# Performance work log

Measured on AMD Instinct MI355X. Metric: run time of the kernel, lower is better.

The kernel has to match this reference:

```python
import jax, jax.numpy as jnp
import numpy as np

H = 16  # num heads
DH = 64  # head dim


def setup_inputs() -> dict:
    key = jax.random.key(0)
    ks = jax.random.split(key, 9)
    d = 1024
    s = 0.02
    return {
        "hidden_states": jax.random.normal(ks[0], (16, 1024, d), jnp.float32),
        "Wq": jax.random.normal(ks[1], (d, d), jnp.float32) * s,
        "bq": jax.random.normal(ks[2], (d,), jnp.float32) * s,
        "Wk": jax.random.normal(ks[3], (d, d), jnp.float32) * s,
        "bk": jax.random.normal(ks[4], (d,), jnp.float32) * s,
        "Wv": jax.random.normal(ks[5], (d, d), jnp.float32) * s,
        "bv": jax.random.normal(ks[6], (d,), jnp.float32) * s,
        "Wo": jax.random.normal(ks[7], (d, d), jnp.float32) * s,
        "bo": jax.random.normal(ks[8], (d,), jnp.float32) * s,
    }


def _heads(x):
    b, s, _ = x.shape
    return x.reshape(b, s, H, DH).transpose(0, 2, 1, 3)  # [B,H,S,Dh]


def reference(hidden_states, Wq, bq, Wk, bk, Wv, bv, Wo, bo):
    # torch nn.Linear: y = x @ W.T + b; weights here are [out, in]
    q = _heads(hidden_states @ Wq.T + bq)
    k = _heads(hidden_states @ Wk.T + bk)
    v = _heads(hidden_states @ Wv.T + bv)
    scores = jnp.einsum("bhqd,bhkd->bhqk", q, k) / jnp.sqrt(jnp.float32(DH))
    probs = jax.nn.softmax(scores, axis=-1)
    ctx = jnp.einsum("bhqk,bhkd->bhqd", probs, v)
    b, _, s, _ = ctx.shape
    ctx = ctx.transpose(0, 2, 1, 3).reshape(b, s, H * DH)
    out = ctx @ Wo.T + bo
    # module returns (attention_output, weights=None); return array only
    return out
```

## Files before the change

kernel.cpp:

```cpp
#include <hip/hip_runtime.h>
#include <hip/hip_bf16.h>
#include <stdint.h>


typedef short bf16x8 __attribute__((ext_vector_type(8)));
typedef float f32x4 __attribute__((ext_vector_type(4)));
typedef float f32x16 __attribute__((ext_vector_type(16)));
typedef unsigned short ushort_t;
typedef ushort_t us8 __attribute__((ext_vector_type(8)));

__device__ __forceinline__ ushort_t f2b(float f) {
    unsigned x;
    __builtin_memcpy(&x, &f, 4);
    unsigned r = (x + 0x7fffu + ((x >> 16) & 1u)) >> 16;
    return (ushort_t)r;
}

__device__ __forceinline__ void glds16(const void* g, void* l) {
    __builtin_amdgcn_global_load_lds(
        (const __attribute__((address_space(1))) void*)g,
        (__attribute__((address_space(3))) void*)l, 16, 0, 0);
}

#define MFMA16(a, b, c) __builtin_amdgcn_mfma_f32_16x16x32_bf16((a), (b), (c), 0, 0, 0)
#define MFMA32(a, b, c) __builtin_amdgcn_mfma_f32_32x32x16_bf16((a), (b), (c), 0, 0, 0)

__global__ __launch_bounds__(256, 8) void cvt4_kernel(
    const float* __restrict__ s0, const float* __restrict__ s1,
    const float* __restrict__ s2, const float* __restrict__ s3,
    ushort_t* __restrict__ d0, ushort_t* __restrict__ d1,
    ushort_t* __restrict__ d2, ushort_t* __restrict__ d3, int n8)
{
    const float* in = (blockIdx.y == 0) ? s0 : (blockIdx.y == 1) ? s1
                       : (blockIdx.y == 2) ? s2 : s3;
    ushort_t* out = (blockIdx.y == 0) ? d0 : (blockIdx.y == 1) ? d1
                       : (blockIdx.y == 2) ? d2 : d3;
    int i = blockIdx.x * 256 + threadIdx.x;
    if (i >= n8) return;
    const float4* p = (const float4*)in + (size_t)i * 2;
    float4 a = p[0], b = p[1];
    us8 v;
    v[0] = f2b(a.x); v[1] = f2b(a.y); v[2] = f2b(a.z); v[3] = f2b(a.w);
    v[4] = f2b(b.x); v[5] = f2b(b.y); v[6] = f2b(b.z); v[7] = f2b(b.w);
    *((us8*)out + i) = v;
}

__global__ __launch_bounds__(256, 8) void cvt1_kernel(
    const float* __restrict__ in, ushort_t* __restrict__ out, int n8)
{
    int i = blockIdx.x * 256 + threadIdx.x;
    if (i >= n8) return;
    const float4* p = (const float4*)in + (size_t)i * 2;
    float4 a = p[0], b = p[1];
    us8 v;
    v[0] = f2b(a.x); v[1] = f2b(a.y); v[2] = f2b(a.z); v[3] = f2b(a.w);
    v[4] = f2b(b.x); v[5] = f2b(b.y); v[6] = f2b(b.z); v[7] = f2b(b.w);
    *((us8*)out + i) = v;
}

template <bool OUTF>
__global__ __launch_bounds__(256, 2) void gemm_bias_kernel(
    const ushort_t* __restrict__ A,
    const ushort_t* __restrict__ W0, const ushort_t* __restrict__ W1, const ushort_t* __restrict__ W2,
    const float* __restrict__ b0, const float* __restrict__ b1, const float* __restrict__ b2,
    void* __restrict__ C0, void* __restrict__ C1, void* __restrict__ C2,
    float s0, float s1, float s2,
    int M, int N, int K)
{
    const ushort_t* W = (blockIdx.z == 0) ? W0 : ((blockIdx.z == 1) ? W1 : W2);
    const float* bias = (blockIdx.z == 0) ? b0 : ((blockIdx.z == 1) ? b1 : b2);
    void* C = (blockIdx.z == 0) ? C0 : ((blockIdx.z == 1) ? C1 : C2);
    const float scale = (blockIdx.z == 0) ? s0 : ((blockIdx.z == 1) ? s1 : s2);

    __shared__ ushort_t As[128 * 64];
    __shared__ ushort_t Bs[128 * 64];

    const int tid = threadIdx.x;
    const int lane = tid & 63;
    const int wave = tid >> 6;
    const int bm = blockIdx.x * 128;
    const int bn = blockIdx.y * 128;
    const int wm = (wave >> 1) * 64;
    const int wn = (wave & 1) * 64;
    const int r32 = lane & 31;
    const int g = lane >> 5;

    f32x16 acc[2][2] = {};

    for (int k0 = 0; k0 < K; k0 += 64) {
        __syncthreads();
#pragma unroll
        for (int it = 0; it < 4; ++it) {
            int cid = it * 256 + tid;
            int r = cid >> 3;
            int s = cid & 7;
            int sc = s ^ (r & 7);
            glds16(A + (size_t)(bm + r) * K + k0 + sc * 8, As + cid * 8);
            glds16(W + (size_t)(bn + r) * K + k0 + sc * 8, Bs + cid * 8);
        }
        __syncthreads();
#pragma unroll
        for (int kk = 0; kk < 4; ++kk) {
            bf16x8 af[2], bfr[2];
#pragma unroll
            for (int i = 0; i < 2; ++i) {
                int row = wm + i * 32 + r32;
                int ch = (kk * 2 + g) ^ (row & 7);
                af[i] = *(const bf16x8*)(As + row * 64 + ch * 8);
                int rowb = wn + i * 32 + r32;
                int chb = (kk * 2 + g) ^ (rowb & 7);
                bfr[i] = *(const bf16x8*)(Bs + rowb * 64 + chb * 8);
            }
#pragma unroll
            for (int i = 0; i < 2; ++i)
#pragma unroll
                for (int j = 0; j < 2; ++j)
                    acc[i][j] = MFMA32(af[i], bfr[j], acc[i][j]);
        }
    }

#pragma unroll
    for (int j = 0; j < 2; ++j) {
        int col = bn + wn + j * 32 + r32;
        float bv = bias[col];
#pragma unroll
        for (int i = 0; i < 2; ++i) {
            int rbase = bm + wm + i * 32 + 4 * g;
#pragma unroll
            for (int reg = 0; reg < 16; ++reg) {
                int row = rbase + (reg & 3) + 8 * (reg >> 2);
                float v = (acc[i][j][reg] + bv) * scale;
                if (OUTF)
                    ((float*)C)[(size_t)row * N + col] = v;
                else
                    ((ushort_t*)C)[(size_t)row * N + col] = f2b(v);
            }
        }
    }
}

__global__ __launch_bounds__(256, 4) void transpose_v_kernel(
    const ushort_t* __restrict__ V, ushort_t* __restrict__ Vt)
{
    __shared__ ushort_t t[64 * 65];
    const int bh = blockIdx.x;
    const int st = blockIdx.y;
    const int b = bh >> 4, h = bh & 15;
    const int tid = threadIdx.x;

#pragma unroll
    for (int i = 0; i < 16; ++i) {
        int e = i * 256 + tid;
        int s = e >> 6, d = e & 63;
        t[s * 65 + d] = V[(size_t)(b * 1024 + st * 64 + s) * 1024 + h * 64 + d];
    }
    __syncthreads();
#pragma unroll
    for (int i = 0; i < 16; ++i) {
        int e = i * 256 + tid;
        int d = e >> 6, s = e & 63;
        Vt[(size_t)(bh * 64 + d) * 1024 + st * 64 + s] = t[s * 65 + d];
    }
}

__global__ __launch_bounds__(256, 4) void attn_kernel(
    const ushort_t* __restrict__ Q, const ushort_t* __restrict__ K,
    const ushort_t* __restrict__ Vt, ushort_t* __restrict__ ctx)
{
    __shared__ ushort_t Ks[64 * 64];
    __shared__ ushort_t Vs[64 * 64];
    __shared__ ushort_t Ps[4][16 * 72];

    const int bh = blockIdx.x;
    const int qt = blockIdx.y;
    const int b = bh >> 4, h = bh & 15;
    const int tid = threadIdx.x;
    const int lane = tid & 63;
    const int wave = tid >> 6;
    const int q = lane >> 4;
    const int ml = lane & 15;

    bf16x8 qf[2][2];
#pragma unroll
    for (int mg = 0; mg < 2; ++mg) {
        int row = b * 1024 + qt * 128 + wave * 32 + mg * 16 + ml;
        const ushort_t* qp = Q + (size_t)row * 1024 + h * 64;
        qf[mg][0] = *(const bf16x8*)(qp + q * 8);
        qf[mg][1] = *(const bf16x8*)(qp + 32 + q * 8);
    }

    f32x4 o[2][4] = {};
    float l[2] = {0.f, 0.f};
    ushort_t* Pw = Ps[wave];

    for (int kt = 0; kt < 16; ++kt) {
        __syncthreads();
#pragma unroll
        for (int it = 0; it < 2; ++it) {
            int cid = it * 256 + tid;
            int r = cid >> 3, s = cid & 7, sc = s ^ (r & 7);
            glds16(K + (size_t)(b * 1024 + kt * 64 + r) * 1024 + h * 64 + sc * 8,
                   Ks + cid * 8);
            glds16(Vt + (size_t)(bh * 64 + r) * 1024 + kt * 64 + sc * 8,
                   Vs + cid * 8);
        }
        __syncthreads();

#pragma unroll
        for (int mg = 0; mg < 2; ++mg) {
#pragma unroll
            for (int n = 0; n < 4; ++n) {
                int row = n * 16 + ml;
                int c0 = q ^ (row & 7);
                int c1 = (4 + q) ^ (row & 7);
                bf16x8 k0 = *(const bf16x8*)(Ks + row * 64 + c0 * 8);
                bf16x8 k1 = *(const bf16x8*)(Ks + row * 64 + c1 * 8);
                f32x4 z = {};
                z = MFMA16(k0, qf[mg][0], z);
                z = MFMA16(k1, qf[mg][1], z);
                float p0 = exp2f(z[0]);
                float p1 = exp2f(z[1]);
                float p2 = exp2f(z[2]);
                float p3 = exp2f(z[3]);
                l[mg] += (p0 + p1) + (p2 + p3);
                __hip_bfloat162 h01 = __float22bfloat162_rn(make_float2(p0, p1));
                __hip_bfloat162 h23 = __float22bfloat162_rn(make_float2(p2, p3));
                uint2 dd;
                __builtin_memcpy(&dd.x, &h01, 4);
                __builtin_memcpy(&dd.y, &h23, 4);
                *(uint2*)(Pw + ml * 72 + n * 16 + q * 4) = dd;
            }

            bf16x8 pf0 = *(const bf16x8*)(Pw + ml * 72 + q * 8);
            bf16x8 pf1 = *(const bf16x8*)(Pw + ml * 72 + 32 + q * 8);

#pragma unroll
            for (int n = 0; n < 4; ++n) {
                int row = n * 16 + ml;
                int c0 = q ^ (row & 7);
                int c1 = (4 + q) ^ (row & 7);
                bf16x8 v0 = *(const bf16x8*)(Vs + row * 64 + c0 * 8);
                bf16x8 v1 = *(const bf16x8*)(Vs + row * 64 + c1 * 8);
                o[mg][n] = MFMA16(pf0, v0, o[mg][n]);
                o[mg][n] = MFMA16(pf1, v1, o[mg][n]);
            }
        }
    }

    float li[2];
#pragma unroll
    for (int mg = 0; mg < 2; ++mg) {
        float s = l[mg];
        s += __shfl_xor(s, 16, 64);
        s += __shfl_xor(s, 32, 64);
        li[mg] = 1.0f / s;
    }

    const int orow_base = b * 1024 + qt * 128 + wave * 32;
#pragma unroll
    for (int mg = 0; mg < 2; ++mg) {
#pragma unroll
        for (int r = 0; r < 4; ++r) {
            float lv = __shfl(li[mg], q * 4 + r, 64);
            int orow = orow_base + mg * 16 + q * 4 + r;
#pragma unroll
            for (int n = 0; n < 4; ++n) {
                ctx[(size_t)orow * 1024 + h * 64 + n * 16 + ml] =
                    f2b(o[mg][n][r] * lv);
            }
        }
    }
}

extern "C" void kernel_launch(void* const* d_in, const int* in_sizes, int n_in,
                              void* d_out, int out_size, void* d_ws, size_t ws_size,
                              hipStream_t stream)
{
    const float* X  = (const float*)d_in[0];
    const float* Wq = (const float*)d_in[1];
    const float* bq = (const float*)d_in[2];
    const float* Wk = (const float*)d_in[3];
    const float* bk = (const float*)d_in[4];
    const float* Wv = (const float*)d_in[5];
    const float* bv = (const float*)d_in[6];
    const float* Wo = (const float*)d_in[7];
    const float* bo = (const float*)d_in[8];

    const int D = 1024;
    const int M = in_sizes[0] / D;
    const int Bb = M / 1024;
    const size_t MD = (size_t)M * D;
    const size_t DD = (size_t)D * D;

    ushort_t* ws  = (ushort_t*)d_ws;
    ushort_t* Xbf = ws;
    ushort_t* Qb  = ws + MD;
    ushort_t* Kb  = ws + 2 * MD;
    ushort_t* Vb  = ws + 3 * MD;
    ushort_t* Wqb = ws + 4 * MD;
    ushort_t* Wkb = Wqb + DD;
    ushort_t* Wvb = Wkb + DD;
    ushort_t* Wob = Wvb + DD;
    ushort_t* Vtb = Xbf;
    ushort_t* ctx = Vb;

    dim3 blk(256);

    cvt1_kernel<<<(int)(MD / 8 / 256), blk, 0, stream>>>(X, Xbf, (int)(MD / 8));
    cvt4_kernel<<<dim3((int)(DD / 8 / 256), 4), blk, 0, stream>>>(
        Wq, Wk, Wv, Wo, Wqb, Wkb, Wvb, Wob, (int)(DD / 8));

    const float qscale = 1.4426950408889634f * 0.125f;
    dim3 gqkv(M / 128, D / 128, 3);
    gemm_bias_kernel<false><<<gqkv, blk, 0, stream>>>(Xbf, Wqb, Wkb, Wvb, bq, bk, bv,
                                                      Qb, Kb, Vb,
                                                      qscale, 1.0f, 1.0f, M, D, D);

    transpose_v_kernel<<<dim3(Bb * 16, 16), blk, 0, stream>>>(Vb, Vtb);

    attn_kernel<<<dim3(Bb * 16, 8), blk, 0, stream>>>(Qb, Kb, Vtb, ctx);

    dim3 go(M / 128, D / 128, 1);
    gemm_bias_kernel<true><<<go, blk, 0, stream>>>(ctx, Wob, Wob, Wob, bo, bo, bo,
                                                   d_out, d_out, d_out,
                                                   1.0f, 1.0f, 1.0f, M, D, D);
}
```

Baseline: 431.8 us.

## Double-buffer K/V tiles in attention and compute row sums with MFMA

The attention kernel now keeps two LDS buffers for the K and V tiles and prefetches the next tile while computing on the current one. This removes one barrier per iteration and hides global-load latency. It also reuses each K fragment load across both query groups and computes the softmax denominator with an MFMA against a ones vector, which drops the shuffle reductions. The exp calls now use the hardware exp2 builtin. LDS use roughly doubles and launch bounds drop to 2 blocks per CU, which lowers occupancy. The denominator is now summed from bf16-rounded probabilities, which slightly changes numerics.

After: 405.6 us. 6.1% less time.

```diff
diff --git a/kernel.cpp b/kernel.cpp
--- a/kernel.cpp
+++ b/kernel.cpp
@@ -163,13 +163,13 @@
     }
 }
 
-__global__ __launch_bounds__(256, 4) void attn_kernel(
+__global__ __launch_bounds__(256, 2) void attn_kernel(
     const ushort_t* __restrict__ Q, const ushort_t* __restrict__ K,
     const ushort_t* __restrict__ Vt, ushort_t* __restrict__ ctx)
 {
-    __shared__ ushort_t Ks[64 * 64];
-    __shared__ ushort_t Vs[64 * 64];
-    __shared__ ushort_t Ps[4][16 * 72];
+    __shared__ ushort_t Ks[2][64 * 64];
+    __shared__ ushort_t Vs[2][64 * 64];
+    __shared__ ushort_t Ps[4][32 * 72];
 
     const int bh = blockIdx.x;
     const int qt = blockIdx.y;
@@ -180,6 +180,13 @@
     const int q = lane >> 4;
     const int ml = lane & 15;
 
+    const int cid0 = tid;
+    const int cid1 = 256 + tid;
+    const int r0 = cid0 >> 3, sc0 = (cid0 & 7) ^ (r0 & 7);
+    const int r1 = cid1 >> 3, sc1 = (cid1 & 7) ^ (r1 & 7);
+    const ushort_t* Kbase = K + (size_t)(b * 1024) * 1024 + h * 64;
+    const ushort_t* Vbase = Vt + (size_t)(bh * 64) * 1024;
+
     bf16x8 qf[2][2];
 #pragma unroll
     for (int mg = 0; mg < 2; ++mg) {
@@ -189,79 +196,83 @@
         qf[mg][1] = *(const bf16x8*)(qp + 32 + q * 8);
     }
 
+    bf16x8 ones;
+#pragma unroll
+    for (int i = 0; i < 8; ++i) ones[i] = (short)0x3F80;
+
     f32x4 o[2][4] = {};
-    float l[2] = {0.f, 0.f};
+    f32x4 ls[2] = {};
     ushort_t* Pw = Ps[wave];
 
+    glds16(Kbase + (size_t)r0 * 1024 + sc0 * 8, Ks[0] + cid0 * 8);
+    glds16(Vbase + (size_t)r0 * 1024 + sc0 * 8, Vs[0] + cid0 * 8);
+    glds16(Kbase + (size_t)r1 * 1024 + sc1 * 8, Ks[0] + cid1 * 8);
+    glds16(Vbase + (size_t)r1 * 1024 + sc1 * 8, Vs[0] + cid1 * 8);
+
     for (int kt = 0; kt < 16; ++kt) {
+        const int cur = kt & 1, nxt = cur ^ 1;
         __syncthreads();
-#pragma unroll
-        for (int it = 0; it < 2; ++it) {
-            int cid = it * 256 + tid;
-            int r = cid >> 3, s = cid & 7, sc = s ^ (r & 7);
-            glds16(K + (size_t)(b * 1024 + kt * 64 + r) * 1024 + h * 64 + sc * 8,
-                   Ks + cid * 8);
-            glds16(Vt + (size_t)(bh * 64 + r) * 1024 + kt * 64 + sc * 8,
-                   Vs + cid * 8);
-        }
-        __syncthreads();
-
-#pragma unroll
-        for (int mg = 0; mg < 2; ++mg) {
-#pragma unroll
-            for (int n = 0; n < 4; ++n) {
-                int row = n * 16 + ml;
-                int c0 = q ^ (row & 7);
-                int c1 = (4 + q) ^ (row & 7);
-                bf16x8 k0 = *(const bf16x8*)(Ks + row * 64 + c0 * 8);
-                bf16x8 k1 = *(const bf16x8*)(Ks + row * 64 + c1 * 8);
+        if (kt + 1 < 16) {
+            const ushort_t* Kn = Kbase + (size_t)(kt + 1) * 64 * 1024;
+            const ushort_t* Vn = Vbase + (kt + 1) * 64;
+            glds16(Kn + (size_t)r0 * 1024 + sc0 * 8, Ks[nxt] + cid0 * 8);
+            glds16(Vn + (size_t)r0 * 1024 + sc0 * 8, Vs[nxt] + cid0 * 8);
+            glds16(Kn + (size_t)r1 * 1024 + sc1 * 8, Ks[nxt] + cid1 * 8);
+            glds16(Vn + (size_t)r1 * 1024 + sc1 * 8, Vs[nxt] + cid1 * 8);
+        }
+        const ushort_t* Kc = Ks[cur];
+        const ushort_t* Vc = Vs[cur];
+
+#pragma unroll
+        for (int n = 0; n < 4; ++n) {
+            int row = n * 16 + ml;
+            int c0 = q ^ (row & 7);
+            int c1 = (4 + q) ^ (row & 7);
+            bf16x8 k0 = *(const bf16x8*)(Kc + row * 64 + c0 * 8);
+            bf16x8 k1 = *(const bf16x8*)(Kc + row * 64 + c1 * 8);
+#pragma unroll
+            for (int mg = 0; mg < 2; ++mg) {
                 f32x4 z = {};
                 z = MFMA16(k0, qf[mg][0], z);
                 z = MFMA16(k1, qf[mg][1], z);
-                float p0 = exp2f(z[0]);
-                float p1 = exp2f(z[1]);
-                float p2 = exp2f(z[2]);
-                float p3 = exp2f(z[3]);
-                l[mg] += (p0 + p1) + (p2 + p3);
+                float p0 = __builtin_amdgcn_exp2f(z[0]);
+                float p1 = __builtin_amdgcn_exp2f(z[1]);
+                float p2 = __builtin_amdgcn_exp2f(z[2]);
+                float p3 = __builtin_amdgcn_exp2f(z[3]);
                 __hip_bfloat162 h01 = __float22bfloat162_rn(make_float2(p0, p1));
                 __hip_bfloat162 h23 = __float22bfloat162_rn(make_float2(p2, p3));
                 uint2 dd;
                 __builtin_memcpy(&dd.x, &h01, 4);
                 __builtin_memcpy(&dd.y, &h23, 4);
-                *(uint2*)(Pw + ml * 72 + n * 16 + q * 4) = dd;
-            }
-
-            bf16x8 pf0 = *(const bf16x8*)(Pw + ml * 72 + q * 8);
-            bf16x8 pf1 = *(const bf16x8*)(Pw + ml * 72 + 32 + q * 8);
-
+                *(uint2*)(Pw + (mg * 16 + ml) * 72 + n * 16 + q * 4) = dd;
+            }
+        }
+
+#pragma unroll
+        for (int mg = 0; mg < 2; ++mg) {
+            bf16x8 pf0 = *(const bf16x8*)(Pw + (mg * 16 + ml) * 72 + q * 8);
+            bf16x8 pf1 = *(const bf16x8*)(Pw + (mg * 16 + ml) * 72 + 32 + q * 8);
+            ls[mg] = MFMA16(pf0, ones, ls[mg]);
+            ls[mg] = MFMA16(pf1, ones, ls[mg]);
 #pragma unroll
             for (int n = 0; n < 4; ++n) {
                 int row = n * 16 + ml;
                 int c0 = q ^ (row & 7);
                 int c1 = (4 + q) ^ (row & 7);
-                bf16x8 v0 = *(const bf16x8*)(Vs + row * 64 + c0 * 8);
-                bf16x8 v1 = *(const bf16x8*)(Vs + row * 64 + c1 * 8);
+                bf16x8 v0 = *(const bf16x8*)(Vc + row * 64 + c0 * 8);
+                bf16x8 v1 = *(const bf16x8*)(Vc + row * 64 + c1 * 8);
                 o[mg][n] = MFMA16(pf0, v0, o[mg][n]);
                 o[mg][n] = MFMA16(pf1, v1, o[mg][n]);
             }
         }
     }
 
-    float li[2];
+    const int orow_base = b * 1024 + qt * 128 + wave * 32;
 #pragma unroll
     for (int mg = 0; mg < 2; ++mg) {
-        float s = l[mg];
-        s += __shfl_xor(s, 16, 64);
-        s += __shfl_xor(s, 32, 64);
-        li[mg] = 1.0f / s;
-    }
-
-    const int orow_base = b * 1024 + qt * 128 + wave * 32;
-#pragma unroll
-    for (int mg = 0; mg < 2; ++mg) {
 #pragma unroll
         for (int r = 0; r < 4; ++r) {
-            float lv = __shfl(li[mg], q * 4 + r, 64);
+            float lv = 1.0f / ls[mg][r];
             int orow = orow_base + mg * 16 + q * 4 + r;
 #pragma unroll
             for (int n = 0; n < 4; ++n) {
```
